# Kernel optimization log

Hardware: AMD Instinct MI355X
Metric: run time of the kernel (lower is better)

Reference implementation:

```python
import jax, jax.numpy as jnp
import numpy as np

HEADS = 16
DIM_HEAD = 64
SCALE = float(np.sqrt(DIM_HEAD))  # NOTE: original code MULTIPLIES by sqrt(dim_head)


def setup_inputs() -> dict:
    key = jax.random.key(0)
    k1, k2, k3, k4 = jax.random.split(key, 4)
    dim = 1024
    b, n = 2, 2048
    s = 1.0 / np.sqrt(dim)
    return {
        "x": jax.random.normal(k1, (b, n, dim), dtype=jnp.float32),
        "w_q": jax.random.normal(k2, (dim, HEADS * DIM_HEAD), dtype=jnp.float32) * s,
        "w_vk": jax.random.normal(k3, (dim, HEADS * DIM_HEAD * 2), dtype=jnp.float32) * s,
        "w_out": jax.random.normal(k4, (HEADS * DIM_HEAD, dim), dtype=jnp.float32) * s,
    }


def reference(x, w_q, w_vk, w_out):
    b, n, _ = x.shape
    h, d = HEADS, DIM_HEAD
    context = x  # context=None, kv_include_self=False
    q = (x @ w_q).reshape(b, n, h, d).transpose(0, 2, 1, 3)          # b h n d
    kv = context @ w_vk                                              # b n 2hd
    k, v = jnp.split(kv, 2, axis=-1)                                 # chunk order: k first, v second
    k = k.reshape(b, n, h, d).transpose(0, 2, 1, 3)
    v = v.reshape(b, n, h, d).transpose(0, 2, 1, 3)
    dots = jnp.einsum('bhid,bhjd->bhij', q, k) * SCALE               # faithful: multiply by sqrt(d)
    attn = jax.nn.softmax(dots, axis=-1)                             # dropout p=0 -> identity
    out = jnp.einsum('bhij,bhjd->bhid', attn, v)
    out = out.transpose(0, 2, 1, 3).reshape(b, n, h * d)
    return out @ w_out
```

## Files before the change

kernel.cpp:

```cpp
#include <hip/hip_runtime.h>

typedef _Float16 half4 __attribute__((ext_vector_type(4)));
typedef _Float16 half8 __attribute__((ext_vector_type(8)));
typedef _Float16 h2pk __attribute__((ext_vector_type(2)));
typedef float f32x4 __attribute__((ext_vector_type(4)));

#define MFMA_F16K32(a, b, c) __builtin_amdgcn_mfma_f32_16x16x32_f16(a, b, c, 0, 0, 0)
#define MFMA_F16K16(a, b, c) __builtin_amdgcn_mfma_f32_16x16x16f16(a, b, c, 0, 0, 0)
#define EXP2F(x) __builtin_amdgcn_exp2f(x)
#define CVT_PK(a, b) __builtin_bit_cast(h2pk, __builtin_amdgcn_cvt_pkrtz(a, b))

constexpr int NSEQ = 2048, DIM = 1024;
constexpr float QSCALE = 11.5415603271f;

__device__ __forceinline__ void ld_lds16(void* lds, const void* g) {
  __builtin_amdgcn_global_load_lds(
      (const __attribute__((address_space(1))) void*)g,
      (__attribute__((address_space(3))) void*)lds, 16, 0, 0);
}

__global__ __launch_bounds__(256) void prep(
    const float* __restrict__ w_q, const float* __restrict__ w_vk,
    const float* __restrict__ w_out, const float* __restrict__ x,
    _Float16* __restrict__ WT, _Float16* __restrict__ WoT,
    _Float16* __restrict__ xf) {
  const int bid = blockIdx.x;
  const int t = threadIdx.x;
  if (bid >= 1024) {
    const size_t i = ((size_t)(bid - 1024) * 256 + t) * 8;
    float4 a = *(const float4*)(x + i), b2 = *(const float4*)(x + i + 4);
    float v[8] = {a.x, a.y, a.z, a.w, b2.x, b2.y, b2.z, b2.w};
    half8 h;
#pragma unroll
    for (int j = 0; j < 8; ++j) h[j] = (_Float16)v[j];
    *(half8*)(xf + i) = h;
    return;
  }
  __shared__ float T[64][65];
  const int bx = bid & 63, k0 = (bid >> 6) * 64;
  const float* src;
  int srcN, n0, dstrow, mode;
  float scale;
  if (bx < 16) {
    src = w_q; srcN = 1024; n0 = bx * 64; dstrow = n0; scale = QSCALE; mode = 0;
  } else if (bx < 48) {
    src = w_vk; srcN = 2048; n0 = (bx - 16) * 64; dstrow = 1024 + n0;
    scale = 1.0f; mode = 0;
  } else {
    src = w_out; srcN = 1024; n0 = (bx - 48) * 64; dstrow = n0;
    scale = 1.0f; mode = 1;
  }
  {
    const int r = t >> 2, c4 = (t & 3) * 16;
    const float* s = src + (size_t)(k0 + r) * srcN + n0 + c4;
    float4 v0 = ((const float4*)s)[0], v1 = ((const float4*)s)[1],
           v2 = ((const float4*)s)[2], v3 = ((const float4*)s)[3];
    *(float4*)&T[r][c4 + 0] = v0;  *(float4*)&T[r][c4 + 4] = v1;
    *(float4*)&T[r][c4 + 8] = v2;  *(float4*)&T[r][c4 + 12] = v3;
  }
  __syncthreads();
  const int rn = t >> 2, kc = (t & 3) * 16;
  half8 hv[2];
#pragma unroll
  for (int hh = 0; hh < 2; ++hh)
#pragma unroll
    for (int j = 0; j < 8; ++j)
      hv[hh][j] = (_Float16)(T[kc + hh * 8 + j][rn] * scale);
  _Float16* d = ((mode == 0) ? WT + (size_t)(dstrow + rn) * 1024
                             : WoT + (size_t)(n0 + rn) * 1024) + k0 + kc;
  *(half8*)d = hv[0]; *(half8*)(d + 8) = hv[1];
}

__global__ __launch_bounds__(256, 4) void proj6(
    const _Float16* __restrict__ xf, const _Float16* __restrict__ WT,
    _Float16* __restrict__ qb, _Float16* __restrict__ kb,
    _Float16* __restrict__ VT) {
  __shared__ __align__(16) char smem[32768];
  const int t = threadIdx.x;
  const int lane = t & 63, wave = t >> 6, quad = lane >> 4, lq = lane & 15;
  const int wid0 = blockIdx.x + 24 * blockIdx.y;
  const int wid = (wid0 & 7) * 96 + (wid0 >> 3);
  const int bn = (wid % 24) * 128, bm = (wid / 24) * 128;
  const int kind = bn >> 10;
  const int wm = (wave >> 1) * 64, wn = (wave & 1) * 64;

  const int srow = lane >> 2;
  const int schk = (lane & 3) ^ (srow & 3);
  const _Float16* xg = xf + (size_t)(bm + wave * 32 + srow) * DIM + schk * 8;
  const _Float16* bg = WT + (size_t)(bn + wave * 32 + srow) * DIM + schk * 8;
  const int wb = wave * 2048;

  auto issue = [&](char* buf, int k0) {
    ld_lds16(buf + wb,                xg + k0);
    ld_lds16(buf + wb + 1024,         xg + k0 + 16 * DIM);
    ld_lds16(buf + 8192 + wb,         bg + k0);
    ld_lds16(buf + 8192 + wb + 1024,  bg + k0 + 16 * DIM);
  };

  const int swz = (quad ^ (lq & 3)) * 8;

  f32x4 acc[4][4];
#pragma unroll
  for (int i = 0; i < 4; ++i)
#pragma unroll
    for (int j = 0; j < 4; ++j) acc[i][j] = (f32x4){0.f, 0.f, 0.f, 0.f};

  char* bufA = smem;
  char* bufB = smem + 16384;
  issue(bufA, 0);
  if (kind == 2) {
    for (int k0 = 0; k0 < DIM; k0 += 32) {
      char* cur = ((k0 >> 5) & 1) ? bufB : bufA;
      char* nxt = ((k0 >> 5) & 1) ? bufA : bufB;
      __syncthreads();
      if (k0 + 32 < DIM) issue(nxt, k0 + 32);
      const _Float16* Xs = (const _Float16*)cur;
      const _Float16* Bs = (const _Float16*)(cur + 8192);
      half8 ah[4];
#pragma unroll
      for (int i = 0; i < 4; ++i)
        ah[i] = *(const half8*)&Xs[(wm + i * 16 + lq) * 32 + swz];
#pragma unroll
      for (int j = 0; j < 4; ++j) {
        half8 bf = *(const half8*)&Bs[(wn + j * 16 + lq) * 32 + swz];
#pragma unroll
        for (int i = 0; i < 4; ++i)
          acc[i][j] = MFMA_F16K32(ah[i], bf, acc[i][j]);
      }
    }
  } else {
    for (int k0 = 0; k0 < DIM; k0 += 32) {
      char* cur = ((k0 >> 5) & 1) ? bufB : bufA;
      char* nxt = ((k0 >> 5) & 1) ? bufA : bufB;
      __syncthreads();
      if (k0 + 32 < DIM) issue(nxt, k0 + 32);
      const _Float16* Xs = (const _Float16*)cur;
      const _Float16* Bs = (const _Float16*)(cur + 8192);
      half8 ah[4];
#pragma unroll
      for (int i = 0; i < 4; ++i)
        ah[i] = *(const half8*)&Xs[(wm + i * 16 + lq) * 32 + swz];
#pragma unroll
      for (int j = 0; j < 4; ++j) {
        half8 bf = *(const half8*)&Bs[(wn + j * 16 + lq) * 32 + swz];
#pragma unroll
        for (int i = 0; i < 4; ++i)
          acc[i][j] = MFMA_F16K32(bf, ah[i], acc[i][j]);
      }
    }
  }

  if (kind == 2) {
    _Float16* Ols = (_Float16*)smem;
    const int cb = bn - 2048;
    __syncthreads();
#pragma unroll
    for (int pass = 0; pass < 2; ++pass) {
      if ((wave >> 1) == pass) {
#pragma unroll
        for (int i = 0; i < 4; ++i)
#pragma unroll
          for (int j = 0; j < 4; ++j) {
            const int c = wn + j * 16 + lq;
            const int tl = i * 16 + quad * 4;
            half4 o;
#pragma unroll
            for (int r = 0; r < 4; ++r) o[r] = (_Float16)acc[i][j][r];
            *(half4*)&Ols[c * 68 + tl] = o;
          }
      }
      __syncthreads();
      {
        const int c = t >> 1, hf = t & 1;
        const int gcol = cb + c;
        const int tok0 = bm + pass * 64 + hf * 32;
        const int b2 = tok0 >> 11, n2 = tok0 & 2047;
        const _Float16* src = &Ols[c * 68 + hf * 32];
        half8 v0 = ((const half8*)src)[0], v1 = ((const half8*)src)[1],
              v2 = ((const half8*)src)[2], v3 = ((const half8*)src)[3];
        _Float16* dst =
            VT + ((size_t)(b2 * 16 + (gcol >> 6)) * 64 + (gcol & 63)) * 2048 + n2;
        ((half8*)dst)[0] = v0; ((half8*)dst)[1] = v1;
        ((half8*)dst)[2] = v2; ((half8*)dst)[3] = v3;
      }
      __syncthreads();
    }
  } else {
    _Float16* D = (kind == 0) ? qb : kb;
    const int cb = bn & 1023;
#pragma unroll
    for (int i = 0; i < 4; ++i) {
      const int row = bm + wm + i * 16 + lq;
#pragma unroll
      for (int j = 0; j < 4; ++j) {
        const int col = cb + wn + j * 16 + quad * 4;
        half4 o;
#pragma unroll
        for (int r = 0; r < 4; ++r) o[r] = (_Float16)acc[i][j][r];
        *(half4*)&D[(size_t)row * 1024 + col] = o;
      }
    }
  }
}

__global__ __launch_bounds__(512, 4) void attn9(
    const _Float16* __restrict__ qb, const _Float16* __restrict__ kb,
    const _Float16* __restrict__ vT, _Float16* __restrict__ ho) {
  __shared__ __align__(16) char smem[65536];
  const int t = threadIdx.x;
  const int lane = t & 63, wave = t >> 6, quad = lane >> 4, lq = lane & 15;
  const int group = wave >> 2, wq = wave & 3;
  const int wid = blockIdx.x + 16 * blockIdx.y;
  const int xcd = wid & 7, slot = wid >> 3;
  const int i0 = (slot & 15) * 128;
  const int bh = xcd + 8 * (slot >> 4);
  const int b = bh >> 4, head = bh & 15;
  const size_t rowbase = (size_t)b * NSEQ;

  half8 qf[2][2];
#pragma unroll
  for (int qt = 0; qt < 2; ++qt) {
    const _Float16* qp =
        qb + (rowbase + i0 + wq * 32 + qt * 16 + lq) * DIM + head * 64 + quad * 8;
    qf[qt][0] = *(const half8*)qp;
    qf[qt][1] = *(const half8*)(qp + 32);
  }

  f32x4 o[2][4];
#pragma unroll
  for (int qt = 0; qt < 2; ++qt)
#pragma unroll
    for (int dt = 0; dt < 4; ++dt) o[qt][dt] = (f32x4){0.f, 0.f, 0.f, 0.f};
  float mrun[2] = {-3.0e38f, -3.0e38f};
  float lrun[2] = {0.f, 0.f};

  const int srow = lane >> 3, schk = (lane & 7) ^ srow;
  const int krow = (wq >> 1) * 32 + (wq & 1) * 4 + ((srow & 4) << 1) + (srow & 3);
  const _Float16* kgp =
      kb + (rowbase + krow) * DIM + head * 64 + schk * 8;
  const int vrow = lane >> 3;
  const int vchk = (lane & 7) ^ vrow;
  const _Float16* vgp =
      vT + ((size_t)bh * 64 + wq * 16 + vrow) * 2048 + vchk * 8;

  auto issue = [&](int bsel, int j) {
    char* kd = smem + (group * 2 + bsel) * 8192 + wq * 2048;
    char* vd = kd + 32768;
    ld_lds16(kd,        kgp + (size_t)(j)      * DIM);
    ld_lds16(kd + 1024, kgp + (size_t)(j + 16) * DIM);
    ld_lds16(vd,        vgp + j);
    ld_lds16(vd + 1024, vgp + 8 * 2048 + j);
  };

  const int swzK0 = (quad ^ (lq & 7)) * 8;
  const int swzK1 = ((quad + 4) ^ (lq & 7)) * 8;

  issue(0, group * 64);

  for (int p = 0; p < 16; ++p) {
    const int cur = p & 1;
    __syncthreads();
    if (p < 15) issue(cur ^ 1, (2 * p + group) * 64 + 128);
    const _Float16* Khs = (const _Float16*)(smem + (group * 2 + cur) * 8192);
    const _Float16* Vts = (const _Float16*)(smem + 32768 + (group * 2 + cur) * 8192);

    f32x4 s[2][4];
    __builtin_amdgcn_s_setprio(1);
#pragma unroll
    for (int nt = 0; nt < 4; ++nt) {
      const int roff = (nt * 16 + lq) * 64;
      half8 k0f = *(const half8*)&Khs[roff + swzK0];
      half8 k1f = *(const half8*)&Khs[roff + swzK1];
#pragma unroll
      for (int qt = 0; qt < 2; ++qt) {
        f32x4 sv = (f32x4){0.f, 0.f, 0.f, 0.f};
        sv = MFMA_F16K32(k0f, qf[qt][0], sv);
        sv = MFMA_F16K32(k1f, qf[qt][1], sv);
        s[qt][nt] = sv;
      }
    }
    __builtin_amdgcn_s_setprio(0);

    half8 pa8[2][2];
#pragma unroll
    for (int qt = 0; qt < 2; ++qt) {
      float m0 = fmaxf(fmaxf(s[qt][0][0], s[qt][0][1]),
                       fmaxf(s[qt][0][2], s[qt][0][3]));
      float m1 = fmaxf(fmaxf(s[qt][1][0], s[qt][1][1]),
                       fmaxf(s[qt][1][2], s[qt][1][3]));
      float m2 = fmaxf(fmaxf(s[qt][2][0], s[qt][2][1]),
                       fmaxf(s[qt][2][2], s[qt][2][3]));
      float m3 = fmaxf(fmaxf(s[qt][3][0], s[qt][3][1]),
                       fmaxf(s[qt][3][2], s[qt][3][3]));
      float mx = fmaxf(fmaxf(m0, m1), fmaxf(m2, m3));
      mx = fmaxf(mx, __shfl_xor(mx, 16));
      mx = fmaxf(mx, __shfl_xor(mx, 32));
      const float mn = fmaxf(mrun[qt], mx);
      const float alpha = EXP2F(mrun[qt] - mn);
      mrun[qt] = mn;
      float rs = 0.f;
#pragma unroll
      for (int nt = 0; nt < 4; ++nt) {
        float p0 = EXP2F(s[qt][nt][0] - mn), p1 = EXP2F(s[qt][nt][1] - mn);
        float p2 = EXP2F(s[qt][nt][2] - mn), p3 = EXP2F(s[qt][nt][3] - mn);
        rs += (p0 + p1) + (p2 + p3);
        h2pk lo = CVT_PK(p0, p1);
        h2pk hi = CVT_PK(p2, p3);
        const int bb = nt >> 1, e = (nt & 1) * 4;
        pa8[qt][bb][e + 0] = lo[0]; pa8[qt][bb][e + 1] = lo[1];
        pa8[qt][bb][e + 2] = hi[0]; pa8[qt][bb][e + 3] = hi[1];
      }
      rs += __shfl_xor(rs, 16);
      rs += __shfl_xor(rs, 32);
      lrun[qt] = lrun[qt] * alpha + rs;
#pragma unroll
      for (int dt = 0; dt < 4; ++dt) o[qt][dt] *= alpha;
    }

    __builtin_amdgcn_s_setprio(1);
#pragma unroll
    for (int dt = 0; dt < 4; ++dt) {
      const int vr2 = (dt * 16 + lq) * 64;
#pragma unroll
      for (int bb = 0; bb < 2; ++bb) {
        const int voff = vr2 + (((bb * 4 + quad) ^ (lq & 7)) * 8);
        half8 va = *(const half8*)&Vts[voff];
        o[0][dt] = MFMA_F16K32(va, pa8[0][bb], o[0][dt]);
        o[1][dt] = MFMA_F16K32(va, pa8[1][bb], o[1][dt]);
      }
    }
    __builtin_amdgcn_s_setprio(0);
  }

  float* dump = (float*)smem;
  __syncthreads();
  if (group == 1) {
    float* D = dump + wq * 2304 + lane * 36;
#pragma unroll
    for (int qt = 0; qt < 2; ++qt)
#pragma unroll
      for (int dt = 0; dt < 4; ++dt)
        *(f32x4*)(D + (qt * 4 + dt) * 4) = o[qt][dt];
    D[32] = mrun[0]; D[33] = lrun[0]; D[34] = mrun[1]; D[35] = lrun[1];
  }
  __syncthreads();
  _Float16* Ots = (_Float16*)(smem + 40960);
  if (group == 0) {
    const float* D = dump + wq * 2304 + lane * 36;
#pragma unroll
    for (int qt = 0; qt < 2; ++qt) {
      const float m2 = D[32 + qt * 2], l2 = D[33 + qt * 2];
      const float mM = fmaxf(mrun[qt], m2);
      const float f1 = EXP2F(mrun[qt] - mM);
      const float f2 = EXP2F(m2 - mM);
      const float inv = 1.0f / (lrun[qt] * f1 + l2 * f2);
#pragma unroll
      for (int dt = 0; dt < 4; ++dt) {
        f32x4 o2 = *(const f32x4*)(D + (qt * 4 + dt) * 4);
#pragma unroll
        for (int r = 0; r < 4; ++r) {
          const float val = (o[qt][dt][r] * f1 + o2[r] * f2) * inv;
          Ots[(wq * 32 + qt * 16 + lq) * 80 + dt * 16 + quad * 4 + r] =
              (_Float16)val;
        }
      }
    }
  }
  __syncthreads();
  {
    const int row = t >> 2, seg = t & 3;
    const _Float16* src = &Ots[row * 80 + seg * 16];
    half8 o0 = ((const half8*)src)[0], o1 = ((const half8*)src)[1];
    _Float16* dst = ho + (rowbase + i0 + row) * DIM + head * 64 + seg * 16;
    ((half8*)dst)[0] = o0; ((half8*)dst)[1] = o1;
  }
}

__global__ __launch_bounds__(256, 4) void gemm_out(
    const _Float16* __restrict__ A, const _Float16* __restrict__ BT,
    float* __restrict__ C) {
  __shared__ __align__(16) char smem[24576];
  const int t = threadIdx.x;
  const int lane = t & 63, wave = t >> 6, quad = lane >> 4, lq = lane & 15;
  const int wid0 = blockIdx.x + 8 * blockIdx.y;
  const int wid = (wid0 & 7) * 64 + (wid0 >> 3);
  const int bn = (wid % 8) * 128, bm = (wid / 8) * 64;
  const int wm = (wave >> 1) * 32, wn = (wave & 1) * 64;

  const int bco = (lane & 7) ^ (lane >> 3);
  const int brow = 2 * (lane >> 3) + (bco >> 2);
  const int bcc = bco & 3;
  const _Float16* ag = A + (size_t)(bm + wave * 16 + brow) * DIM + bcc * 8;
  const _Float16* bg = BT + (size_t)(bn + wave * 32 + brow) * DIM + bcc * 8;
  const int swzB = ((((lq & 1) << 2) | quad) ^ ((lq >> 1) & 7)) * 8;

  auto issue = [&](char* buf, int k0) {
    ld_lds16(buf + wave * 1024,               ag + k0);
    ld_lds16(buf + 4096 + wave * 2048,        bg + k0);
    ld_lds16(buf + 4096 + wave * 2048 + 1024, bg + k0 + 16 * DIM);
  };

  f32x4 acc[2][4];
#pragma unroll
  for (int i = 0; i < 2; ++i)
#pragma unroll
    for (int j = 0; j < 4; ++j) acc[i][j] = (f32x4){0.f, 0.f, 0.f, 0.f};

  char* bufA = smem;
  char* bufB = smem + 12288;
  issue(bufA, 0);
  for (int k0 = 0; k0 < DIM; k0 += 32) {
    char* cur = ((k0 >> 5) & 1) ? bufB : bufA;
    char* nxt = ((k0 >> 5) & 1) ? bufA : bufB;
    __syncthreads();
    if (k0 + 32 < DIM) issue(nxt, k0 + 32);
    const _Float16* Ahs = (const _Float16*)cur;
    const _Float16* Bhs = (const _Float16*)(cur + 4096);
    half8 ah[2];
#pragma unroll
    for (int i = 0; i < 2; ++i) {
      const int row = wm + i * 16 + lq;
      ah[i] = *(const half8*)&Ahs[(row >> 1) * 64 + swzB];
    }
#pragma unroll
    for (int j = 0; j < 4; ++j) {
      const int row = wn + j * 16 + lq;
      half8 bf = *(const half8*)&Bhs[(row >> 1) * 64 + swzB];
#pragma unroll
      for (int i = 0; i < 2; ++i)
        acc[i][j] = MFMA_F16K32(bf, ah[i], acc[i][j]);
    }
  }
#pragma unroll
  for (int i = 0; i < 2; ++i) {
    const int row = bm + wm + i * 16 + lq;
#pragma unroll
    for (int j = 0; j < 4; ++j) {
      const int col = bn + wn + j * 16 + quad * 4;
      *(f32x4*)&C[(size_t)row * 1024 + col] = acc[i][j];
    }
  }
}

extern "C" void kernel_launch(void* const* d_in, const int* in_sizes, int n_in,
                              void* d_out, int out_size, void* d_ws,
                              size_t ws_size, hipStream_t stream) {
  const float* x     = (const float*)d_in[0];
  const float* w_q   = (const float*)d_in[1];
  const float* w_vk  = (const float*)d_in[2];
  const float* w_out = (const float*)d_in[3];
  float* out = (float*)d_out;

  char* w = (char*)d_ws;
  _Float16* wT  = (_Float16*)(w);
  _Float16* woT = (_Float16*)(w + (6ull << 20));
  _Float16* qbb = (_Float16*)(w + (8ull << 20));
  _Float16* kbb = (_Float16*)(w + (16ull << 20));
  _Float16* vTb = (_Float16*)(w + (24ull << 20));
  _Float16* hob = (_Float16*)(w + (32ull << 20));
  _Float16* xfb = (_Float16*)(w + (40ull << 20));

  dim3 blk(256);
  prep<<<dim3(3072), blk, 0, stream>>>(w_q, w_vk, w_out, x, wT, woT, xfb);
  proj6<<<dim3(24, 32), blk, 0, stream>>>(xfb, wT, qbb, kbb, vTb);
  attn9<<<dim3(16, 32), dim3(512), 0, stream>>>(qbb, kbb, vTb, hob);
  gemm_out<<<dim3(8, 64), blk, 0, stream>>>(hob, woT, out);
}
```

Baseline: 180.1 us.

## Software-pipeline attention: compute next tile's QK^T before current PV

Restructures the attention main loop so the QK^T MFMAs for tile p+1 are issued after the softmax of tile p and before its PV MFMAs. The aim is to overlap exp/softmax VALU work with matrix-core work, and to prefetch two tiles ahead. K stays double-buffered, V becomes triple-buffered, and LDS grows from 64KB to 80KB per block. This can lower occupancy (launch bounds ask for 4 waves per SIMD) and adds register pressure from keeping the score tile live across iterations.

```diff
diff --git a/kernel.cpp b/kernel.cpp
--- a/kernel.cpp
+++ b/kernel.cpp
@@ -6,7 +6,6 @@
 typedef float f32x4 __attribute__((ext_vector_type(4)));
 
 #define MFMA_F16K32(a, b, c) __builtin_amdgcn_mfma_f32_16x16x32_f16(a, b, c, 0, 0, 0)
-#define MFMA_F16K16(a, b, c) __builtin_amdgcn_mfma_f32_16x16x16f16(a, b, c, 0, 0, 0)
 #define EXP2F(x) __builtin_amdgcn_exp2f(x)
 #define CVT_PK(a, b) __builtin_bit_cast(h2pk, __builtin_amdgcn_cvt_pkrtz(a, b))
 
@@ -203,10 +202,10 @@
   }
 }
 
-__global__ __launch_bounds__(512, 4) void attn9(
+__global__ __launch_bounds__(512, 4) void attn10(
     const _Float16* __restrict__ qb, const _Float16* __restrict__ kb,
     const _Float16* __restrict__ vT, _Float16* __restrict__ ho) {
-  __shared__ __align__(16) char smem[65536];
+  __shared__ __align__(16) char smem[81920];
   const int t = threadIdx.x;
   const int lane = t & 63, wave = t >> 6, quad = lane >> 4, lq = lane & 15;
   const int group = wave >> 2, wq = wave & 3;
@@ -243,11 +242,19 @@
   const _Float16* vgp =
       vT + ((size_t)bh * 64 + wq * 16 + vrow) * 2048 + vchk * 8;
 
-  auto issue = [&](int bsel, int j) {
-    char* kd = smem + (group * 2 + bsel) * 8192 + wq * 2048;
-    char* vd = kd + 32768;
-    ld_lds16(kd,        kgp + (size_t)(j)      * DIM);
+  char* gb = smem + group * 40960;
+  char* kbf0 = gb;          char* kbf1 = gb + 8192;
+  char* vbf0 = gb + 16384;  char* vbf1 = gb + 24576;  char* vbf2 = gb + 32768;
+
+  auto issueK = [&](char* buf, int tile) {
+    const int j = (2 * tile + group) * 64;
+    char* kd = buf + wq * 2048;
+    ld_lds16(kd,        kgp + (size_t)j * DIM);
     ld_lds16(kd + 1024, kgp + (size_t)(j + 16) * DIM);
+  };
+  auto issueV = [&](char* buf, int tile) {
+    const int j = (2 * tile + group) * 64;
+    char* vd = buf + wq * 2048;
     ld_lds16(vd,        vgp + j);
     ld_lds16(vd + 1024, vgp + 8 * 2048 + j);
   };
@@ -255,16 +262,9 @@
   const int swzK0 = (quad ^ (lq & 7)) * 8;
   const int swzK1 = ((quad + 4) ^ (lq & 7)) * 8;
 
-  issue(0, group * 64);
-
-  for (int p = 0; p < 16; ++p) {
-    const int cur = p & 1;
-    __syncthreads();
-    if (p < 15) issue(cur ^ 1, (2 * p + group) * 64 + 128);
-    const _Float16* Khs = (const _Float16*)(smem + (group * 2 + cur) * 8192);
-    const _Float16* Vts = (const _Float16*)(smem + 32768 + (group * 2 + cur) * 8192);
-
-    f32x4 s[2][4];
+  f32x4 s[2][4];
+  auto QKT = [&](const char* kbuf) {
+    const _Float16* Khs = (const _Float16*)kbuf;
     __builtin_amdgcn_s_setprio(1);
 #pragma unroll
     for (int nt = 0; nt < 4; ++nt) {
@@ -280,6 +280,22 @@
       }
     }
     __builtin_amdgcn_s_setprio(0);
+  };
+
+  issueK(kbf0, 0); issueV(vbf0, 0);
+  __syncthreads();
+  issueK(kbf1, 1); issueV(vbf1, 1);
+  QKT(kbf0);
+
+  char* kbufs[2] = {kbf0, kbf1};
+  char* vbufs[3] = {vbf0, vbf1, vbf2};
+
+  for (int p = 0; p < 16; ++p) {
+    __syncthreads();
+    if (p <= 13) {
+      issueK(kbufs[p & 1], p + 2);
+      issueV(vbufs[(p + 2) % 3], p + 2);
+    }
 
     half8 pa8[2][2];
 #pragma unroll
@@ -317,19 +333,24 @@
       for (int dt = 0; dt < 4; ++dt) o[qt][dt] *= alpha;
     }
 
-    __builtin_amdgcn_s_setprio(1);
-#pragma unroll
-    for (int dt = 0; dt < 4; ++dt) {
-      const int vr2 = (dt * 16 + lq) * 64;
-#pragma unroll
-      for (int bb = 0; bb < 2; ++bb) {
-        const int voff = vr2 + (((bb * 4 + quad) ^ (lq & 7)) * 8);
-        half8 va = *(const half8*)&Vts[voff];
-        o[0][dt] = MFMA_F16K32(va, pa8[0][bb], o[0][dt]);
-        o[1][dt] = MFMA_F16K32(va, pa8[1][bb], o[1][dt]);
-      }
-    }
-    __builtin_amdgcn_s_setprio(0);
+    if (p <= 14) QKT(kbufs[(p + 1) & 1]);
+
+    {
+      const _Float16* Vts = (const _Float16*)vbufs[p % 3];
+      __builtin_amdgcn_s_setprio(1);
+#pragma unroll
+      for (int dt = 0; dt < 4; ++dt) {
+        const int vr2 = (dt * 16 + lq) * 64;
+#pragma unroll
+        for (int bb = 0; bb < 2; ++bb) {
+          const int voff = vr2 + (((bb * 4 + quad) ^ (lq & 7)) * 8);
+          half8 va = *(const half8*)&Vts[voff];
+          o[0][dt] = MFMA_F16K32(va, pa8[0][bb], o[0][dt]);
+          o[1][dt] = MFMA_F16K32(va, pa8[1][bb], o[1][dt]);
+        }
+      }
+      __builtin_amdgcn_s_setprio(0);
+    }
   }
 
   float* dump = (float*)smem;
@@ -463,6 +484,6 @@
   dim3 blk(256);
   prep<<<dim3(3072), blk, 0, stream>>>(w_q, w_vk, w_out, x, wT, woT, xfb);
   proj6<<<dim3(24, 32), blk, 0, stream>>>(xfb, wT, qbb, kbb, vTb);
-  attn9<<<dim3(16, 32), dim3(512), 0, stream>>>(qbb, kbb, vTb, hob);
+  attn10<<<dim3(16, 32), dim3(512), 0, stream>>>(qbb, kbb, vTb, hob);
   gemm_out<<<dim3(8, 64), blk, 0, stream>>>(hob, woT, out);
 }
```

New measurement: 350.0 us. 94.3% more time.
